# Optimization experiments

Hardware: AMD Instinct MI355X
Metric: run time of the kernel (lower is better)

Reference implementation:

```python
import jax, jax.numpy as jnp
import numpy as np

N_NODES = 100000
D_IN = 128
D_OUT = 128
B, T, S = 8, 4096, 25


def setup_inputs() -> dict:
    key = jax.random.key(0)
    k1, k2, k3 = jax.random.split(key, 3)
    features = jax.random.normal(k1, (N_NODES, D_IN), dtype=jnp.float32)
    sample_res = jax.random.randint(k2, (B, T, S), 0, N_NODES, dtype=jnp.int64)
    # glorot-uniform init for [D_IN, D_OUT]
    limit = np.sqrt(6.0 / (D_IN + D_OUT)).astype(np.float32)
    weights = jax.random.uniform(k3, (D_IN, D_OUT), dtype=jnp.float32,
                                 minval=-limit, maxval=limit)
    return {"features": features, "sample_res": sample_res, "weights": weights}


def reference(features, sample_res, weights):
    # gather neighbor embeddings: [B, T, S, D]
    sampled = features[sample_res]
    # mean over sampled-neighbor axis -> [B, T, D]
    neigh_vecs = jnp.mean(sampled, axis=2)
    # shared linear transform + relu (bias=False per init defaults)
    out = jnp.einsum('btd,do->bto', neigh_vecs, weights)
    return jax.nn.relu(out)
```

## Files before the change

kernel.cpp:

```cpp
#include <hip/hip_runtime.h>


#define DEG 25
#define DIM 128
#define NPP 25000

typedef __attribute__((ext_vector_type(8))) short short8;
typedef __attribute__((ext_vector_type(4))) float floatx4;
typedef __attribute__((ext_vector_type(4))) unsigned int uintx4;

__device__ __forceinline__ unsigned short f2bf(float f) {
    unsigned u = __float_as_uint(f);
    return (unsigned short)((u + 0x7fffu + ((u >> 16) & 1u)) >> 16);
}

#define BSTRIDE 136

__global__ __launch_bounds__(256, 2) void gemm_fw(
    const float* __restrict__ A,
    const float* __restrict__ B,
    unsigned short* __restrict__ G,
    int M)
{
    __shared__ unsigned short sBt[DIM * BSTRIDE];

    const int tid = threadIdx.x;

    {
        const float4* B4 = (const float4*)B;
#pragma unroll
        for (int i = 0; i < 16; ++i) {
            const int linear = i * 256 + tid;
            const int k  = linear >> 5;
            const int c4 = linear & 31;
            const float4 v = B4[linear];
            const int n = c4 * 4;
            sBt[(n + 0) * BSTRIDE + k] = f2bf(v.x);
            sBt[(n + 1) * BSTRIDE + k] = f2bf(v.y);
            sBt[(n + 2) * BSTRIDE + k] = f2bf(v.z);
            sBt[(n + 3) * BSTRIDE + k] = f2bf(v.w);
        }
    }
    __syncthreads();

    const int wave = tid >> 6;
    const int lane = tid & 63;
    const int quad = lane >> 4;
    const int l16  = lane & 15;

    const int rw0 = blockIdx.x * 128 + wave * 32;

    floatx4 acc[2][8];
#pragma unroll
    for (int mt = 0; mt < 2; ++mt)
#pragma unroll
        for (int nt = 0; nt < 8; ++nt)
            acc[mt][nt] = (floatx4){0.f, 0.f, 0.f, 0.f};

#pragma unroll
    for (int kt = 0; kt < 4; ++kt) {
        const int k0 = kt * 32;

        short8 afrag[2];
#pragma unroll
        for (int mt = 0; mt < 2; ++mt) {
            int row = rw0 + mt * 16 + l16;
            if (row >= M) row = M - 1;
            const float* ap = A + (size_t)row * DIM + k0 + quad * 8;
            const float4 x = *(const float4*)ap;
            const float4 y = *(const float4*)(ap + 4);
            unsigned p0 = (unsigned)f2bf(x.x) | ((unsigned)f2bf(x.y) << 16);
            unsigned p1 = (unsigned)f2bf(x.z) | ((unsigned)f2bf(x.w) << 16);
            unsigned p2 = (unsigned)f2bf(y.x) | ((unsigned)f2bf(y.y) << 16);
            unsigned p3 = (unsigned)f2bf(y.z) | ((unsigned)f2bf(y.w) << 16);
            uintx4 packed = (uintx4){p0, p1, p2, p3};
            afrag[mt] = __builtin_bit_cast(short8, packed);
        }

#pragma unroll
        for (int nt = 0; nt < 8; ++nt) {
            const uintx4 u = *(const uintx4*)&sBt[(nt * 16 + l16) * BSTRIDE + k0 + quad * 8];
            const short8 bfrag = __builtin_bit_cast(short8, u);
#pragma unroll
            for (int mt = 0; mt < 2; ++mt)
                acc[mt][nt] = __builtin_amdgcn_mfma_f32_16x16x32_bf16(
                    afrag[mt], bfrag, acc[mt][nt], 0, 0, 0);
        }
    }

    __syncthreads();
    {
        unsigned short* sT = sBt + wave * (32 * BSTRIDE);
#pragma unroll
        for (int mt = 0; mt < 2; ++mt)
#pragma unroll
            for (int nt = 0; nt < 8; ++nt)
#pragma unroll
                for (int r = 0; r < 4; ++r)
                    sT[(mt * 16 + quad * 4 + r) * BSTRIDE + nt * 16 + l16] =
                        f2bf(acc[mt][nt][r]);
    }
    __syncthreads();
    {
        const unsigned short* sT = sBt + wave * (32 * BSTRIDE);
        const int oct   = lane & 7;
        const int nrow8 = lane >> 3;
        uintx4* G4 = (uintx4*)G;
#pragma unroll
        for (int g = 0; g < 4; ++g) {
            const int lrow = g * 8 + nrow8;
            const int node = rw0 + lrow;
            if (node < M) {
                const unsigned p     = (unsigned)node / NPP;
                const unsigned local = (unsigned)node - p * NPP;
#pragma unroll
                for (int h = 0; h < 2; ++h) {
                    const uintx4 u = *(const uintx4*)
                        &sT[lrow * BSTRIDE + h * 64 + oct * 8];
                    __builtin_nontemporal_store(u,
                        &G4[((size_t)(p * 2 + h) * NPP + local) * 8 + oct]);
                }
            }
        }
    }
}

#define GRB 32

__global__ __launch_bounds__(256, 4) void gather_phased(
    const unsigned short* __restrict__ G,
    const int* __restrict__ idx,
    float* __restrict__ out,
    int n_rows)
{
    __shared__ int sRaw[GRB * DEG];
    __shared__ int sOrd[GRB][DEG];
    __shared__ int sCnt[GRB][4];

    const int tid  = threadIdx.x;
    const int h    = blockIdx.x & 1;
    const int rb   = blockIdx.x >> 1;
    const int row0 = rb * GRB;

    const int* ib = idx + (size_t)row0 * DEG;
    for (int i = tid; i < GRB * DEG; i += 256)
        sRaw[i] = __builtin_nontemporal_load(ib + i);
    __syncthreads();

    if (tid < GRB * 4) {
        const int row = tid >> 2;
        const int rg  = tid & 3;
        const int lo  = rg * NPP;
        int cnt = 0;
#pragma unroll
        for (int s = 0; s < DEG; ++s) {
            const unsigned d = (unsigned)(sRaw[row * DEG + s] - lo);
            cnt += (d < NPP) ? 1 : 0;
        }
        sCnt[row][rg] = cnt;
    }
    __syncthreads();

    if (tid < GRB * 4) {
        const int row = tid >> 2;
        const int rg  = tid & 3;
        const int lo  = rg * NPP;
        int off = 0;
        for (int q = 0; q < 4; ++q) off += (q < rg) ? sCnt[row][q] : 0;
        const int base = (rg * 2 + h) * NPP - lo;
#pragma unroll
        for (int s = 0; s < DEG; ++s) {
            const int raw = sRaw[row * DEG + s];
            const unsigned d = (unsigned)(raw - lo);
            if (d < NPP) sOrd[row][off++] = raw + base;
        }
    }
    __syncthreads();

    const int oct = tid & 7;
    const int r   = tid >> 3;
    const uintx4* __restrict__ G4 = (const uintx4*)G + oct;

    uintx4 v[DEG];
#pragma unroll
    for (int s = 0; s < DEG; ++s)
        v[s] = G4[(size_t)sOrd[r][s] * 8];

    float a0 = 0.f, a1 = 0.f, a2 = 0.f, a3 = 0.f;
    float a4 = 0.f, a5 = 0.f, a6 = 0.f, a7 = 0.f;
#pragma unroll
    for (int s = 0; s < DEG; ++s) {
        a0 += __uint_as_float(v[s].x << 16);
        a1 += __uint_as_float(v[s].x & 0xffff0000u);
        a2 += __uint_as_float(v[s].y << 16);
        a3 += __uint_as_float(v[s].y & 0xffff0000u);
        a4 += __uint_as_float(v[s].z << 16);
        a5 += __uint_as_float(v[s].z & 0xffff0000u);
        a6 += __uint_as_float(v[s].w << 16);
        a7 += __uint_as_float(v[s].w & 0xffff0000u);
    }

    const float inv = 1.0f / 25.0f;
    floatx4* op = (floatx4*)(out + (size_t)(row0 + r) * DIM + h * 64 + oct * 8);
    const floatx4 o0 = {fmaxf(a0 * inv, 0.f), fmaxf(a1 * inv, 0.f),
                        fmaxf(a2 * inv, 0.f), fmaxf(a3 * inv, 0.f)};
    const floatx4 o1 = {fmaxf(a4 * inv, 0.f), fmaxf(a5 * inv, 0.f),
                        fmaxf(a6 * inv, 0.f), fmaxf(a7 * inv, 0.f)};
    __builtin_nontemporal_store(o0, op);
    __builtin_nontemporal_store(o1, op + 1);
}

#define RPB 16
#define CG 32

__device__ __forceinline__ float4 relu4(float4 v) {
    return make_float4(fmaxf(v.x, 0.f), fmaxf(v.y, 0.f),
                       fmaxf(v.z, 0.f), fmaxf(v.w, 0.f));
}

__global__ __launch_bounds__(256, 4) void gcn_fused(
    const float* __restrict__ F, const int* __restrict__ idx,
    const float* __restrict__ W, float* __restrict__ out, int n_rows)
{
    __shared__ float4 sV[RPB * CG];
    __shared__ int    sIdx[RPB * DEG];

    const float4* F4 = (const float4*)F;
    const float4* W4 = (const float4*)W;
    float4* out4 = (float4*)out;

    const int tid = threadIdx.x;
    const int row0 = blockIdx.x * RPB;

    for (int i = tid; i < RPB * DEG; i += 256)
        sIdx[i] = idx[(size_t)row0 * DEG + i];
    __syncthreads();

    const int cg = tid & 31;
    const int rs = tid >> 5;

#pragma unroll
    for (int rr = 0; rr < 2; ++rr) {
        const int r = rs + rr * 8;
        int j[DEG];
#pragma unroll
        for (int s = 0; s < DEG; ++s) j[s] = sIdx[r * DEG + s];
        float4 acc = make_float4(0.f, 0.f, 0.f, 0.f);
#pragma unroll
        for (int s = 0; s < DEG; ++s) {
            float4 f = F4[(size_t)j[s] * CG + cg];
            acc.x += f.x; acc.y += f.y; acc.z += f.z; acc.w += f.w;
        }
        const float inv = 1.0f / 25.0f;
        acc.x *= inv; acc.y *= inv; acc.z *= inv; acc.w *= inv;
        sV[r * CG + cg] = acc;
    }
    __syncthreads();

    const float4* vA = &sV[rs * CG];
    const float4* vB = &sV[(rs + 8) * CG];
    float4 o0 = make_float4(0.f, 0.f, 0.f, 0.f);
    float4 o1 = make_float4(0.f, 0.f, 0.f, 0.f);
#pragma unroll 4
    for (int d4 = 0; d4 < CG; ++d4) {
        const float4 a = vA[d4];
        const float4 b = vB[d4];
        const float4 w0 = W4[(size_t)(4 * d4 + 0) * CG + cg];
        const float4 w1 = W4[(size_t)(4 * d4 + 1) * CG + cg];
        const float4 w2 = W4[(size_t)(4 * d4 + 2) * CG + cg];
        const float4 w3 = W4[(size_t)(4 * d4 + 3) * CG + cg];
        o0.x += a.x*w0.x + a.y*w1.x + a.z*w2.x + a.w*w3.x;
        o0.y += a.x*w0.y + a.y*w1.y + a.z*w2.y + a.w*w3.y;
        o0.z += a.x*w0.z + a.y*w1.z + a.z*w2.z + a.w*w3.z;
        o0.w += a.x*w0.w + a.y*w1.w + a.z*w2.w + a.w*w3.w;
        o1.x += b.x*w0.x + b.y*w1.x + b.z*w2.x + b.w*w3.x;
        o1.y += b.x*w0.y + b.y*w1.y + b.z*w2.y + b.w*w3.y;
        o1.z += b.x*w0.z + b.y*w1.z + b.z*w2.z + b.w*w3.z;
        o1.w += b.x*w0.w + b.y*w1.w + b.z*w2.w + b.w*w3.w;
    }
    out4[(size_t)(row0 + rs) * CG + cg]     = relu4(o0);
    out4[(size_t)(row0 + rs + 8) * CG + cg] = relu4(o1);
}

extern "C" void kernel_launch(void* const* d_in, const int* in_sizes, int n_in,
                              void* d_out, int out_size, void* d_ws, size_t ws_size,
                              hipStream_t stream) {
    const float* F   = (const float*)d_in[0];
    const int*   idx = (const int*)d_in[1];
    const float* W   = (const float*)d_in[2];
    float* out = (float*)d_out;

    const int n_nodes = in_sizes[0] / DIM;
    const int n_rows  = in_sizes[1] / DEG;

    const size_t need = (size_t)8 * NPP * 64 * sizeof(unsigned short);

    if (n_nodes == 100000 && ws_size >= need && (n_rows & (GRB - 1)) == 0) {
        unsigned short* G = (unsigned short*)d_ws;
        gemm_fw<<<(n_nodes + 127) / 128, 256, 0, stream>>>(F, W, G, n_nodes);
        gather_phased<<<(n_rows / GRB) * 2, 256, 0, stream>>>(G, idx, out, n_rows);
    } else {
        gcn_fused<<<n_rows / RPB, 256, 0, stream>>>(F, idx, W, out, n_rows);
    }
}
```

Before: 132.5 us.

## Phase bf16 gather by node partition with cooperative grid syncs

```diff
diff --git a/kernel.cpp b/kernel.cpp
--- a/kernel.cpp
+++ b/kernel.cpp
@@ -1,4 +1,7 @@
 #include <hip/hip_runtime.h>
+#include <hip/hip_cooperative_groups.h>
+
+namespace cg = cooperative_groups;
 
 
 #define DEG 25
@@ -125,8 +128,9 @@
     }
 }
 
-#define GRB 32
-
+#define GRB 64
+
+template <bool GSYNC>
 __global__ __launch_bounds__(256, 4) void gather_phased(
     const unsigned short* __restrict__ G,
     const int* __restrict__ idx,
@@ -136,6 +140,7 @@
     __shared__ int sRaw[GRB * DEG];
     __shared__ int sOrd[GRB][DEG];
     __shared__ int sCnt[GRB][4];
+    __shared__ int sStart[GRB][5];
 
     const int tid  = threadIdx.x;
     const int h    = blockIdx.x & 1;
@@ -147,7 +152,7 @@
         sRaw[i] = __builtin_nontemporal_load(ib + i);
     __syncthreads();
 
-    if (tid < GRB * 4) {
+    {
         const int row = tid >> 2;
         const int rg  = tid & 3;
         const int lo  = rg * NPP;
@@ -161,13 +166,15 @@
     }
     __syncthreads();
 
-    if (tid < GRB * 4) {
+    {
         const int row = tid >> 2;
         const int rg  = tid & 3;
         const int lo  = rg * NPP;
         int off = 0;
         for (int q = 0; q < 4; ++q) off += (q < rg) ? sCnt[row][q] : 0;
-        const int base = (rg * 2 + h) * NPP - lo;
+        sStart[row][rg] = off;
+        if (rg == 0) sStart[row][4] = DEG;
+        const int base = (rg + h) * NPP;
 #pragma unroll
         for (int s = 0; s < DEG; ++s) {
             const int raw = sRaw[row * DEG + s];
@@ -178,36 +185,64 @@
     __syncthreads();
 
     const int oct = tid & 7;
-    const int r   = tid >> 3;
+    const int rsl = tid >> 3;
     const uintx4* __restrict__ G4 = (const uintx4*)G + oct;
 
-    uintx4 v[DEG];
-#pragma unroll
-    for (int s = 0; s < DEG; ++s)
-        v[s] = G4[(size_t)sOrd[r][s] * 8];
-
-    float a0 = 0.f, a1 = 0.f, a2 = 0.f, a3 = 0.f;
-    float a4 = 0.f, a5 = 0.f, a6 = 0.f, a7 = 0.f;
-#pragma unroll
-    for (int s = 0; s < DEG; ++s) {
-        a0 += __uint_as_float(v[s].x << 16);
-        a1 += __uint_as_float(v[s].x & 0xffff0000u);
-        a2 += __uint_as_float(v[s].y << 16);
-        a3 += __uint_as_float(v[s].y & 0xffff0000u);
-        a4 += __uint_as_float(v[s].z << 16);
-        a5 += __uint_as_float(v[s].z & 0xffff0000u);
-        a6 += __uint_as_float(v[s].w << 16);
-        a7 += __uint_as_float(v[s].w & 0xffff0000u);
-    }
+    float acc[2][8];
+#pragma unroll
+    for (int rr = 0; rr < 2; ++rr)
+#pragma unroll
+        for (int j = 0; j < 8; ++j) acc[rr][j] = 0.f;
+
+#define ACC8(rr, v)                                       \
+    do {                                                  \
+        acc[rr][0] += __uint_as_float((v).x << 16);       \
+        acc[rr][1] += __uint_as_float((v).x & 0xffff0000u); \
+        acc[rr][2] += __uint_as_float((v).y << 16);       \
+        acc[rr][3] += __uint_as_float((v).y & 0xffff0000u); \
+        acc[rr][4] += __uint_as_float((v).z << 16);       \
+        acc[rr][5] += __uint_as_float((v).z & 0xffff0000u); \
+        acc[rr][6] += __uint_as_float((v).w << 16);       \
+        acc[rr][7] += __uint_as_float((v).w & 0xffff0000u); \
+    } while (0)
+
+    for (int p = 0; p < 4; ++p) {
+#pragma unroll
+        for (int rr = 0; rr < 2; ++rr) {
+            const int r  = rsl + rr * 32;
+            const int c1 = sStart[r][p + 1];
+            const int* lp = &sOrd[r][0];
+            int i = sStart[r][p];
+            for (; i + 4 <= c1; i += 4) {
+                const uintx4 v0 = G4[(size_t)lp[i + 0] * 8];
+                const uintx4 v1 = G4[(size_t)lp[i + 1] * 8];
+                const uintx4 v2 = G4[(size_t)lp[i + 2] * 8];
+                const uintx4 v3 = G4[(size_t)lp[i + 3] * 8];
+                ACC8(rr, v0); ACC8(rr, v1); ACC8(rr, v2); ACC8(rr, v3);
+            }
+            for (; i < c1; ++i) {
+                const uintx4 v = G4[(size_t)lp[i] * 8];
+                ACC8(rr, v);
+            }
+        }
+        if constexpr (GSYNC) {
+            if (p < 3) cg::this_grid().sync();
+        }
+    }
+#undef ACC8
 
     const float inv = 1.0f / 25.0f;
-    floatx4* op = (floatx4*)(out + (size_t)(row0 + r) * DIM + h * 64 + oct * 8);
-    const floatx4 o0 = {fmaxf(a0 * inv, 0.f), fmaxf(a1 * inv, 0.f),
-                        fmaxf(a2 * inv, 0.f), fmaxf(a3 * inv, 0.f)};
-    const floatx4 o1 = {fmaxf(a4 * inv, 0.f), fmaxf(a5 * inv, 0.f),
-                        fmaxf(a6 * inv, 0.f), fmaxf(a7 * inv, 0.f)};
-    __builtin_nontemporal_store(o0, op);
-    __builtin_nontemporal_store(o1, op + 1);
+#pragma unroll
+    for (int rr = 0; rr < 2; ++rr) {
+        const int r = rsl + rr * 32;
+        floatx4* op = (floatx4*)(out + (size_t)(row0 + r) * DIM + h * 64 + oct * 8);
+        const floatx4 o0 = {fmaxf(acc[rr][0] * inv, 0.f), fmaxf(acc[rr][1] * inv, 0.f),
+                            fmaxf(acc[rr][2] * inv, 0.f), fmaxf(acc[rr][3] * inv, 0.f)};
+        const floatx4 o1 = {fmaxf(acc[rr][4] * inv, 0.f), fmaxf(acc[rr][5] * inv, 0.f),
+                            fmaxf(acc[rr][6] * inv, 0.f), fmaxf(acc[rr][7] * inv, 0.f)};
+        __builtin_nontemporal_store(o0, op);
+        __builtin_nontemporal_store(o1, op + 1);
+    }
 }
 
 #define RPB 16
@@ -236,7 +271,7 @@
         sIdx[i] = idx[(size_t)row0 * DEG + i];
     __syncthreads();
 
-    const int cg = tid & 31;
+    const int cg32 = tid & 31;
     const int rs = tid >> 5;
 
 #pragma unroll
@@ -248,12 +283,12 @@
         float4 acc = make_float4(0.f, 0.f, 0.f, 0.f);
 #pragma unroll
         for (int s = 0; s < DEG; ++s) {
-            float4 f = F4[(size_t)j[s] * CG + cg];
+            float4 f = F4[(size_t)j[s] * CG + cg32];
             acc.x += f.x; acc.y += f.y; acc.z += f.z; acc.w += f.w;
         }
         const float inv = 1.0f / 25.0f;
         acc.x *= inv; acc.y *= inv; acc.z *= inv; acc.w *= inv;
-        sV[r * CG + cg] = acc;
+        sV[r * CG + cg32] = acc;
     }
     __syncthreads();
 
@@ -265,10 +300,10 @@
     for (int d4 = 0; d4 < CG; ++d4) {
         const float4 a = vA[d4];
         const float4 b = vB[d4];
-        const float4 w0 = W4[(size_t)(4 * d4 + 0) * CG + cg];
-        const float4 w1 = W4[(size_t)(4 * d4 + 1) * CG + cg];
-        const float4 w2 = W4[(size_t)(4 * d4 + 2) * CG + cg];
-        const float4 w3 = W4[(size_t)(4 * d4 + 3) * CG + cg];
+        const float4 w0 = W4[(size_t)(4 * d4 + 0) * CG + cg32];
+        const float4 w1 = W4[(size_t)(4 * d4 + 1) * CG + cg32];
+        const float4 w2 = W4[(size_t)(4 * d4 + 2) * CG + cg32];
+        const float4 w3 = W4[(size_t)(4 * d4 + 3) * CG + cg32];
         o0.x += a.x*w0.x + a.y*w1.x + a.z*w2.x + a.w*w3.x;
         o0.y += a.x*w0.y + a.y*w1.y + a.z*w2.y + a.w*w3.y;
         o0.z += a.x*w0.z + a.y*w1.z + a.z*w2.z + a.w*w3.z;
@@ -278,8 +313,8 @@
         o1.z += b.x*w0.z + b.y*w1.z + b.z*w2.z + b.w*w3.z;
         o1.w += b.x*w0.w + b.y*w1.w + b.z*w2.w + b.w*w3.w;
     }
-    out4[(size_t)(row0 + rs) * CG + cg]     = relu4(o0);
-    out4[(size_t)(row0 + rs + 8) * CG + cg] = relu4(o1);
+    out4[(size_t)(row0 + rs) * CG + cg32]     = relu4(o0);
+    out4[(size_t)(row0 + rs + 8) * CG + cg32] = relu4(o1);
 }
 
 extern "C" void kernel_launch(void* const* d_in, const int* in_sizes, int n_in,
@@ -291,14 +326,23 @@
     float* out = (float*)d_out;
 
     const int n_nodes = in_sizes[0] / DIM;
-    const int n_rows  = in_sizes[1] / DEG;
+    int n_rows  = in_sizes[1] / DEG;
 
     const size_t need = (size_t)8 * NPP * 64 * sizeof(unsigned short);
 
     if (n_nodes == 100000 && ws_size >= need && (n_rows & (GRB - 1)) == 0) {
         unsigned short* G = (unsigned short*)d_ws;
         gemm_fw<<<(n_nodes + 127) / 128, 256, 0, stream>>>(F, W, G, n_nodes);
-        gather_phased<<<(n_rows / GRB) * 2, 256, 0, stream>>>(G, idx, out, n_rows);
+
+        const int nb = (n_rows / GRB) * 2;
+        const unsigned short* Gc = G;
+        void* args[] = {(void*)&Gc, (void*)&idx, (void*)&out, (void*)&n_rows};
+        hipError_t e = hipLaunchCooperativeKernel(
+            (const void*)(&gather_phased<true>), dim3(nb), dim3(256),
+            args, 0, stream);
+        if (e != hipSuccess) {
+            gather_phased<false><<<nb, 256, 0, stream>>>(G, idx, out, n_rows);
+        }
     } else {
         gcn_fused<<<n_rows / RPB, 256, 0, stream>>>(F, idx, W, out, n_rows);
     }
```

Result: slower. 455.0 us (+243.4%).
